# Performance work log

Hardware: AMD Instinct MI355X
Metric: run time of the kernel (lower is better)

Reference implementation:

```python
import jax, jax.numpy as jnp
import numpy as np

D_OUT, D1, D2 = 512, 512, 512
R0, R1, R2 = 128, 128, 128
BATCH = 8192


def setup_inputs() -> dict:
    key = jax.random.key(0)
    k1, k2, k3, k4, k5, k6 = jax.random.split(key, 6)
    return {
        "X1": jax.random.normal(k1, (D1, BATCH), dtype=jnp.float32),
        "X2": jax.random.normal(k2, (D2, BATCH), dtype=jnp.float32),
        "U0": jax.random.normal(k3, (D_OUT, R0), dtype=jnp.float32) * 0.05,
        "U1": jax.random.normal(k4, (D1, R1), dtype=jnp.float32) * 0.05,
        "U2": jax.random.normal(k5, (D2, R2), dtype=jnp.float32) * 0.05,
        "G": jax.random.normal(k6, (R0, R1, R2), dtype=jnp.float32) * 0.05,
    }


def reference(X1, X2, U0, U1, U2, G):
    # Per-mode projections: UX_i = U_{i+1}^T @ X_i  -> [r_i, B]
    UX1 = U1.T @ X1  # [R1, B]
    UX2 = U2.T @ X2  # [R2, B]
    # Column-wise Khatri-Rao product of UX1, UX2 gives kron per column with
    # row index q*R2 + r (C order), which matches mode-0 unfolding of G.
    # Fused form: core = G_(0) @ khatri_rao(UX1, UX2), expressed as one einsum.
    core = jnp.einsum('pqr,qb,rb->pb', G, UX1, UX2)  # [R0, B]
    Z = U0 @ core  # [D_OUT, B]
    return Z
```

## Files before the change

### kernel.cpp

```cpp
#include <hip/hip_runtime.h>
#include <hip/hip_bf16.h>
#include <stdint.h>


typedef __attribute__((ext_vector_type(8))) short bf8;
typedef __attribute__((ext_vector_type(4))) short bf4;
typedef __attribute__((ext_vector_type(4))) float f4;

__device__ __forceinline__ unsigned short f2bf(float f){
  unsigned x = __builtin_bit_cast(unsigned, f);
  x += 0x7fffu + ((x >> 16) & 1u);
  return (unsigned short)(x >> 16);
}
__device__ __forceinline__ float bf2f(unsigned short u){
  unsigned x = ((unsigned)u) << 16;
  return __builtin_bit_cast(float, x);
}
__device__ __forceinline__ void glds16(const void* g, void* l){
  __builtin_amdgcn_global_load_lds(
      (const __attribute__((address_space(1))) void*)g,
      (__attribute__((address_space(3))) void*)l, 16, 0, 0);
}

__global__ __launch_bounds__(256) void k_cast(const float* __restrict__ G,
                                              const float* __restrict__ U0,
                                              const float* __restrict__ U1,
                                              const float* __restrict__ U2,
                                              unsigned short* __restrict__ Gbf,
                                              unsigned short* __restrict__ U0bf,
                                              unsigned short* __restrict__ U1T,
                                              unsigned short* __restrict__ U2T){
  const int blk = blockIdx.x;
  if (blk < 2112){
    const int i4 = blk * 256 + threadIdx.x;
    const int NG4 = 2097152 / 4;
    const float4* src; unsigned short* dst; int j4;
    if (i4 < NG4){ src = (const float4*)G;  dst = Gbf;  j4 = i4; }
    else         { src = (const float4*)U0; dst = U0bf; j4 = i4 - NG4; }
    float4 v = src[j4];
    ushort4 o = make_ushort4(f2bf(v.x), f2bf(v.y), f2bf(v.z), f2bf(v.w));
    ((ushort4*)dst)[j4] = o;
  } else {
    const int b2 = blk - 2112;
    const float* U = (b2 < 256) ? U1 : U2;
    unsigned short* UT = (b2 < 256) ? U1T : U2T;
    const int idx = (b2 & 255) * 256 + threadIdx.x;
    const int d = idx >> 7, q = idx & 127;
    UT[q * 512 + d] = f2bf(U[idx]);
  }
}

__global__ __launch_bounds__(256) void k_ux2(const unsigned short* __restrict__ U1T,
                                             const unsigned short* __restrict__ U2T,
                                             const float* __restrict__ X1,
                                             const float* __restrict__ X2,
                                             float* __restrict__ OUTF,
                                             unsigned short* __restrict__ OUTT){
  const bool second = (blockIdx.y != 0);
  const unsigned short* UT = second ? U2T : U1T;
  const float* X = second ? X2 : X1;
  __shared__ __align__(16) unsigned char lds[16384 + 8192];
  unsigned char* ldsA = lds;
  unsigned char* ldsB = lds + 16384;
  const int tid = threadIdx.x, lane = tid & 63, wv = tid >> 6;
  const int wr = wv >> 1, wc = wv & 1;
  const int b0 = blockIdx.x * 64;
  f4 acc[4][2] = {};

  for (int it = 0; it < 8; ++it){
    const int k0 = it * 64;
#pragma unroll
    for (int i = 0; i < 4; ++i){
      const int L = (wv * 4 + i) * 1024 + lane * 16;
      const int row = L >> 7;
      const int ss = (lane & 7) ^ (row & 7);
      glds16(UT + (size_t)row * 512 + k0 + ss * 8, ldsA + (wv * 4 + i) * 1024);
    }
#pragma unroll
    for (int c = 0; c < 2; ++c){
      const int slot = c * 4 + wv;
      const int bRow = lane;
      bf8 v;
#pragma unroll
      for (int j = 0; j < 8; ++j)
        v[j] = (short)f2bf(X[(size_t)(k0 + slot * 8 + j) * 8192 + b0 + bRow]);
      *(bf8*)(ldsB + bRow * 128 + ((slot ^ (bRow & 7)) << 4)) = v;
    }
    __syncthreads();
#pragma unroll
    for (int kc = 0; kc < 2; ++kc){
      const int g = lane >> 4;
      bf8 a[4], b[2];
#pragma unroll
      for (int mf = 0; mf < 4; ++mf){
        const int r = wr * 64 + mf * 16 + (lane & 15);
        a[mf] = *(const bf8*)(ldsA + r * 128 + (((kc * 4 + g) ^ (r & 7)) << 4));
      }
#pragma unroll
      for (int nf = 0; nf < 2; ++nf){
        const int rb = wc * 32 + nf * 16 + (lane & 15);
        b[nf] = *(const bf8*)(ldsB + rb * 128 + (((kc * 4 + g) ^ (rb & 7)) << 4));
      }
#pragma unroll
      for (int mf = 0; mf < 4; ++mf)
#pragma unroll
        for (int nf = 0; nf < 2; ++nf)
          acc[mf][nf] = __builtin_amdgcn_mfma_f32_16x16x32_bf16(a[mf], b[nf], acc[mf][nf], 0, 0, 0);
    }
    __syncthreads();
  }

  if (!second){
#pragma unroll
    for (int mf = 0; mf < 4; ++mf)
#pragma unroll
      for (int nf = 0; nf < 2; ++nf)
#pragma unroll
        for (int j = 0; j < 4; ++j){
          const int q = wr * 64 + mf * 16 + (lane >> 4) * 4 + j;
          const int b = b0 + wc * 32 + nf * 16 + (lane & 15);
          OUTF[(size_t)q * 8192 + b] = acc[mf][nf][j];
        }
  } else {
#pragma unroll
    for (int mf = 0; mf < 4; ++mf)
#pragma unroll
      for (int nf = 0; nf < 2; ++nf){
        const int rBase = wr * 64 + mf * 16 + (lane >> 4) * 4;
        const int bL = wc * 32 + nf * 16 + (lane & 15);
        bf4 p;
#pragma unroll
        for (int j = 0; j < 4; ++j) p[j] = (short)f2bf(acc[mf][nf][j]);
        *(bf4*)(lds + ((bL * 256 + rBase * 2) ^ ((bL & 7) << 4))) = p;
      }
    __syncthreads();
#pragma unroll
    for (int u = 0; u < 4; ++u){
      const int sIdx = u * 256 + tid;
      const int bL = sIdx >> 4, slot = sIdx & 15;
      bf8 v = *(const bf8*)(lds + bL * 256 + ((slot ^ (bL & 7)) << 4));
      *(bf8*)(OUTT + (size_t)(b0 + bL) * 128 + slot * 8) = v;
    }
  }
}

__global__ __launch_bounds__(512, 2) void k_core(const unsigned short* __restrict__ Gbf,
                                                 const float* __restrict__ UX1,
                                                 const unsigned short* __restrict__ UX2T,
                                                 unsigned short* __restrict__ PT){
  __shared__ __align__(16) unsigned char lds[147456];
  unsigned char* ldsX = lds + 131072;
  const int tid = threadIdx.x, lane = tid & 63, wv = tid >> 6;
  const int g = lane >> 4, l15 = lane & 15;
  const int wr = wv >> 1, wc = wv & 1;
  const int blk = blockIdx.x;
  const int xcd = blk & 7, slot = blk >> 3;
  const int split = xcd >> 1;
  const int b0 = ((xcd & 1) * 32 + slot) * 128;
  const int q0 = split * 32;

  auto stageA = [&](int q, int buf){
#pragma unroll
    for (int rnd = 0; rnd < 4; ++rnd){
      const int off = rnd * 8192 + wv * 1024 + lane * 16;
      const int row = off >> 8;
      const int ss = ((off >> 4) & 15) ^ (row & 7);
      glds16(Gbf + (size_t)row * 16384 + (size_t)q * 128 + ss * 8,
             lds + buf * 32768 + off);
    }
  };

#pragma unroll
  for (int rnd = 0; rnd < 2; ++rnd){
    const int off = rnd * 8192 + wv * 1024 + lane * 16;
    const int row = off >> 9;
    glds16(UX1 + (size_t)(q0 + row) * 8192 + b0 + ((off >> 2) & 127), ldsX + off);
  }
  bf8 Bf[4][4];
#pragma unroll
  for (int kc = 0; kc < 4; ++kc)
#pragma unroll
    for (int nf = 0; nf < 4; ++nf)
      Bf[kc][nf] = *(const bf8*)(UX2T + (size_t)(b0 + wc * 64 + nf * 16 + l15) * 128 +
                                 kc * 32 + g * 8);
  stageA(q0 + 0, 0);
  stageA(q0 + 1, 1);
  stageA(q0 + 2, 2);

  f4 acc[2][4];
#pragma unroll
  for (int mf = 0; mf < 2; ++mf)
#pragma unroll
    for (int nf = 0; nf < 4; ++nf) acc[mf][nf] = (f4){0.f, 0.f, 0.f, 0.f};

  auto bodyq = [&](int i){
    const unsigned char* A = lds + (i & 3) * 32768;
    float xs[4];
#pragma unroll
    for (int nf = 0; nf < 4; ++nf)
      xs[nf] = *(const float*)(ldsX + i * 512 + (wc * 64 + nf * 16 + l15) * 4);
    bf8 a[2][4];
#pragma unroll
    for (int mf = 0; mf < 2; ++mf){
      const int row = wr * 32 + mf * 16 + l15;
#pragma unroll
      for (int kc = 0; kc < 4; ++kc)
        a[mf][kc] = *(const bf8*)(A + row * 256 + ((((kc << 2) + g) ^ (row & 7)) << 4));
    }
#pragma unroll
    for (int mf = 0; mf < 2; ++mf)
#pragma unroll
      for (int nf = 0; nf < 4; ++nf){
        f4 y = __builtin_amdgcn_mfma_f32_16x16x32_bf16(a[mf][0], Bf[0][nf], (f4){0.f,0.f,0.f,0.f}, 0, 0, 0);
        y = __builtin_amdgcn_mfma_f32_16x16x32_bf16(a[mf][1], Bf[1][nf], y, 0, 0, 0);
        y = __builtin_amdgcn_mfma_f32_16x16x32_bf16(a[mf][2], Bf[2][nf], y, 0, 0, 0);
        y = __builtin_amdgcn_mfma_f32_16x16x32_bf16(a[mf][3], Bf[3][nf], y, 0, 0, 0);
        acc[mf][nf] += y * xs[nf];
      }
  };

  for (int i = 0; i < 30; ++i){
    asm volatile("s_waitcnt vmcnt(8)" ::: "memory");
    __builtin_amdgcn_s_barrier();
    stageA(q0 + i + 3, (i + 3) & 3);
    bodyq(i);
  }
  asm volatile("s_waitcnt vmcnt(4)" ::: "memory");
  __builtin_amdgcn_s_barrier();
  bodyq(30);
  asm volatile("s_waitcnt vmcnt(0)" ::: "memory");
  __builtin_amdgcn_s_barrier();
  bodyq(31);

  __syncthreads();
#pragma unroll
  for (int mf = 0; mf < 2; ++mf)
#pragma unroll
    for (int nf = 0; nf < 4; ++nf){
      const int bL = wc * 64 + nf * 16 + l15;
      const int pq = wr * 8 + mf * 4 + g;
      *(f4*)(lds + bL * 512 + ((pq ^ (bL & 7)) << 4)) = acc[mf][nf];
    }
  __syncthreads();
#pragma unroll
  for (int rnd = 0; rnd < 4; ++rnd){
    const int idx = rnd * 512 + tid;
    const int bL = idx >> 4, s8 = idx & 15;
    f4 lo = *(const f4*)(lds + bL * 512 + (((s8 * 2) ^ (bL & 7)) << 4));
    f4 hi = *(const f4*)(lds + bL * 512 + (((s8 * 2 + 1) ^ (bL & 7)) << 4));
    bf8 o;
#pragma unroll
    for (int j = 0; j < 4; ++j){
      o[j] = (short)f2bf(lo[j]);
      o[4 + j] = (short)f2bf(hi[j]);
    }
    *(bf8*)(PT + (size_t)split * 1048576 + (size_t)(b0 + bL) * 128 + s8 * 8) = o;
  }
}

__global__ __launch_bounds__(256) void k_red(const unsigned short* __restrict__ PT,
                                             unsigned short* __restrict__ coreT){
  const int c = blockIdx.x * 256 + threadIdx.x;
  const bf8* P = (const bf8*)PT;
  bf8 v0 = P[c], v1 = P[c + 131072], v2 = P[c + 262144], v3 = P[c + 393216];
  bf8 o;
#pragma unroll
  for (int j = 0; j < 8; ++j){
    float s = bf2f((unsigned short)v0[j]) + bf2f((unsigned short)v1[j]) +
              bf2f((unsigned short)v2[j]) + bf2f((unsigned short)v3[j]);
    o[j] = (short)f2bf(s);
  }
  ((bf8*)coreT)[c] = o;
}

__global__ __launch_bounds__(256) void k_z(const unsigned short* __restrict__ U0bf,
                                           const unsigned short* __restrict__ coreT,
                                           float* __restrict__ Z){
  __shared__ __align__(16) unsigned char lds[32768];
  unsigned char* ldsA = lds;
  unsigned char* ldsB = lds + 16384;
  const int tid = threadIdx.x, lane = tid & 63, wv = tid >> 6;
  const int wr = wv >> 1, wc = wv & 1;
  const int b0 = blockIdx.x * 128;
  const int d0 = blockIdx.y * 128;
  f4 acc[4][4] = {};

#pragma unroll
  for (int it = 0; it < 2; ++it){
    const int k0 = it * 64;
#pragma unroll
    for (int i = 0; i < 4; ++i){
      const int L = (wv * 4 + i) * 1024 + lane * 16;
      const int row = L >> 7;
      const int ss = (lane & 7) ^ (row & 7);
      glds16(U0bf + (size_t)(d0 + row) * 128 + k0 + ss * 8, ldsA + (wv * 4 + i) * 1024);
      glds16(coreT + (size_t)(b0 + row) * 128 + k0 + ss * 8, ldsB + (wv * 4 + i) * 1024);
    }
    __syncthreads();
#pragma unroll
    for (int kc = 0; kc < 2; ++kc){
      const int g = lane >> 4;
      bf8 a[4], b[4];
#pragma unroll
      for (int mf = 0; mf < 4; ++mf){
        const int r = wr * 64 + mf * 16 + (lane & 15);
        a[mf] = *(const bf8*)(ldsA + r * 128 + (((kc * 4 + g) ^ (r & 7)) << 4));
      }
#pragma unroll
      for (int nf = 0; nf < 4; ++nf){
        const int rb = wc * 64 + nf * 16 + (lane & 15);
        b[nf] = *(const bf8*)(ldsB + rb * 128 + (((kc * 4 + g) ^ (rb & 7)) << 4));
      }
#pragma unroll
      for (int mf = 0; mf < 4; ++mf)
#pragma unroll
        for (int nf = 0; nf < 4; ++nf)
          acc[mf][nf] = __builtin_amdgcn_mfma_f32_16x16x32_bf16(a[mf], b[nf], acc[mf][nf], 0, 0, 0);
    }
    __syncthreads();
  }
#pragma unroll
  for (int mf = 0; mf < 4; ++mf)
#pragma unroll
    for (int nf = 0; nf < 4; ++nf)
#pragma unroll
      for (int j = 0; j < 4; ++j){
        const int d = d0 + wr * 64 + mf * 16 + (lane >> 4) * 4 + j;
        const int b = b0 + wc * 64 + nf * 16 + (lane & 15);
        Z[(size_t)d * 8192 + b] = acc[mf][nf][j];
      }
}

extern "C" void kernel_launch(void* const* d_in, const int* in_sizes, int n_in,
                              void* d_out, int out_size, void* d_ws, size_t ws_size,
                              hipStream_t stream){
  const float* X1 = (const float*)d_in[0];
  const float* X2 = (const float*)d_in[1];
  const float* U0 = (const float*)d_in[2];
  const float* U1 = (const float*)d_in[3];
  const float* U2 = (const float*)d_in[4];
  const float* G  = (const float*)d_in[5];
  float* Z = (float*)d_out;

  char* ws = (char*)d_ws;
  unsigned short* Gbf   = (unsigned short*)(ws);
  unsigned short* U0bf  = (unsigned short*)(ws + 4194304);
  unsigned short* U1T   = (unsigned short*)(ws + 4325376);
  unsigned short* U2T   = (unsigned short*)(ws + 4456448);
  float*          UX1   = (float*)         (ws + 4587520);
  unsigned short* UX2T  = (unsigned short*)(ws + 8781824);
  unsigned short* coreT = (unsigned short*)(ws + 10878976);
  unsigned short* PT    = (unsigned short*)(ws + 12976128);

  k_cast<<<dim3(2624), dim3(256), 0, stream>>>(G, U0, U1, U2, Gbf, U0bf, U1T, U2T);
  k_ux2 <<<dim3(128, 2), dim3(256), 0, stream>>>(U1T, U2T, X1, X2, UX1, UX2T);
  k_core<<<dim3(256), dim3(512), 0, stream>>>(Gbf, UX1, UX2T, PT);
  k_red <<<dim3(512), dim3(256), 0, stream>>>(PT, coreT);
  k_z   <<<dim3(64, 4), dim3(256), 0, stream>>>(U0bf, coreT, Z);
}
```

Baseline: 70.06 us.

## Give each core wave a private G ring, drop block barriers, split q eightfold

Restructures k_core so each of 4 waves owns 32 rows of p and stages its own double-buffered G slices. This removes the block-wide s_barrier from every q step, and UX1 scalars are read straight from global memory instead of an LDS stage. The q range is split across 8 blocks instead of 4, giving 512 smaller blocks with less LDS each. Partials are rounded to bf16 before the LDS transpose, and k_red now sums 8 partial buffers. The cost is double the partial-sum write and reduce traffic, a larger PT workspace, and an extra bf16 rounding step on the partials.

```diff
diff --git a/kernel.cpp b/kernel.cpp
--- a/kernel.cpp
+++ b/kernel.cpp
@@ -144,73 +144,68 @@
   }
 }
 
-__global__ __launch_bounds__(512, 2) void k_core(const unsigned short* __restrict__ Gbf,
+__global__ __launch_bounds__(256, 2) void k_core(const unsigned short* __restrict__ Gbf,
                                                  const float* __restrict__ UX1,
                                                  const unsigned short* __restrict__ UX2T,
                                                  unsigned short* __restrict__ PT){
-  __shared__ __align__(16) unsigned char lds[147456];
-  unsigned char* ldsX = lds + 131072;
+  __shared__ __align__(16) unsigned char lds[65536];
   const int tid = threadIdx.x, lane = tid & 63, wv = tid >> 6;
   const int g = lane >> 4, l15 = lane & 15;
-  const int wr = wv >> 1, wc = wv & 1;
   const int blk = blockIdx.x;
-  const int xcd = blk & 7, slot = blk >> 3;
-  const int split = xcd >> 1;
-  const int b0 = ((xcd & 1) * 32 + slot) * 128;
-  const int q0 = split * 32;
+  const int split = blk & 7;
+  const int b0 = (blk >> 3) * 128;
+  const int q0 = split * 16;
+  const int p0 = wv * 32;
+  unsigned char* ring = lds + wv * 16384;
 
   auto stageA = [&](int q, int buf){
-#pragma unroll
-    for (int rnd = 0; rnd < 4; ++rnd){
-      const int off = rnd * 8192 + wv * 1024 + lane * 16;
-      const int row = off >> 8;
-      const int ss = ((off >> 4) & 15) ^ (row & 7);
-      glds16(Gbf + (size_t)row * 16384 + (size_t)q * 128 + ss * 8,
-             lds + buf * 32768 + off);
+    unsigned char* dst = ring + buf * 8192;
+#pragma unroll
+    for (int j = 0; j < 8; ++j){
+      const int row = j * 4 + g;
+      const int ss = l15 ^ (row & 7);
+      glds16(Gbf + (size_t)(p0 + row) * 16384 + (size_t)q * 128 + ss * 8,
+             dst + j * 1024);
     }
   };
 
-#pragma unroll
-  for (int rnd = 0; rnd < 2; ++rnd){
-    const int off = rnd * 8192 + wv * 1024 + lane * 16;
-    const int row = off >> 9;
-    glds16(UX1 + (size_t)(q0 + row) * 8192 + b0 + ((off >> 2) & 127), ldsX + off);
-  }
-  bf8 Bf[4][4];
+  bf8 Bf[4][8];
 #pragma unroll
   for (int kc = 0; kc < 4; ++kc)
 #pragma unroll
-    for (int nf = 0; nf < 4; ++nf)
-      Bf[kc][nf] = *(const bf8*)(UX2T + (size_t)(b0 + wc * 64 + nf * 16 + l15) * 128 +
+    for (int nf = 0; nf < 8; ++nf)
+      Bf[kc][nf] = *(const bf8*)(UX2T + (size_t)(b0 + nf * 16 + l15) * 128 +
                                  kc * 32 + g * 8);
   stageA(q0 + 0, 0);
   stageA(q0 + 1, 1);
-  stageA(q0 + 2, 2);
-
-  f4 acc[2][4];
+
+  f4 acc[2][8];
 #pragma unroll
   for (int mf = 0; mf < 2; ++mf)
 #pragma unroll
-    for (int nf = 0; nf < 4; ++nf) acc[mf][nf] = (f4){0.f, 0.f, 0.f, 0.f};
-
-  auto bodyq = [&](int i){
-    const unsigned char* A = lds + (i & 3) * 32768;
-    float xs[4];
-#pragma unroll
-    for (int nf = 0; nf < 4; ++nf)
-      xs[nf] = *(const float*)(ldsX + i * 512 + (wc * 64 + nf * 16 + l15) * 4);
+    for (int nf = 0; nf < 8; ++nf) acc[mf][nf] = (f4){0.f, 0.f, 0.f, 0.f};
+
+  auto iter = [&](int i, bool stage_next){
+    const unsigned char* A = ring + (i & 1) * 8192;
+    float xs[8];
+#pragma unroll
+    for (int nf = 0; nf < 8; ++nf)
+      xs[nf] = UX1[(size_t)(q0 + i) * 8192 + b0 + nf * 16 + l15];
     bf8 a[2][4];
 #pragma unroll
     for (int mf = 0; mf < 2; ++mf){
-      const int row = wr * 32 + mf * 16 + l15;
+      const int row = mf * 16 + l15;
 #pragma unroll
       for (int kc = 0; kc < 4; ++kc)
         a[mf][kc] = *(const bf8*)(A + row * 256 + ((((kc << 2) + g) ^ (row & 7)) << 4));
     }
+    asm volatile("s_waitcnt lgkmcnt(0)" ::: "memory");
+    __builtin_amdgcn_sched_barrier(0);
+    if (stage_next) stageA(q0 + i + 2, i & 1);
 #pragma unroll
     for (int mf = 0; mf < 2; ++mf)
 #pragma unroll
-      for (int nf = 0; nf < 4; ++nf){
+      for (int nf = 0; nf < 8; ++nf){
         f4 y = __builtin_amdgcn_mfma_f32_16x16x32_bf16(a[mf][0], Bf[0][nf], (f4){0.f,0.f,0.f,0.f}, 0, 0, 0);
         y = __builtin_amdgcn_mfma_f32_16x16x32_bf16(a[mf][1], Bf[1][nf], y, 0, 0, 0);
         y = __builtin_amdgcn_mfma_f32_16x16x32_bf16(a[mf][2], Bf[2][nf], y, 0, 0, 0);
@@ -219,41 +214,37 @@
       }
   };
 
-  for (int i = 0; i < 30; ++i){
+  for (int i = 0; i < 14; ++i){
     asm volatile("s_waitcnt vmcnt(8)" ::: "memory");
-    __builtin_amdgcn_s_barrier();
-    stageA(q0 + i + 3, (i + 3) & 3);
-    bodyq(i);
-  }
-  asm volatile("s_waitcnt vmcnt(4)" ::: "memory");
-  __builtin_amdgcn_s_barrier();
-  bodyq(30);
+    iter(i, true);
+  }
+  asm volatile("s_waitcnt vmcnt(8)" ::: "memory");
+  iter(14, false);
   asm volatile("s_waitcnt vmcnt(0)" ::: "memory");
-  __builtin_amdgcn_s_barrier();
-  bodyq(31);
+  iter(15, false);
 
   __syncthreads();
 #pragma unroll
   for (int mf = 0; mf < 2; ++mf)
 #pragma unroll
-    for (int nf = 0; nf < 4; ++nf){
-      const int bL = wc * 64 + nf * 16 + l15;
-      const int pq = wr * 8 + mf * 4 + g;
-      *(f4*)(lds + bL * 512 + ((pq ^ (bL & 7)) << 4)) = acc[mf][nf];
+    for (int nf = 0; nf < 8; ++nf){
+      const int bL = nf * 16 + l15;
+      const int pq = wv * 8 + mf * 4 + g;
+      bf4 o;
+#pragma unroll
+      for (int j = 0; j < 4; ++j) o[j] = (short)f2bf(acc[mf][nf][j]);
+      *(bf4*)(lds + bL * 256 + ((pq ^ (bL & 7)) << 3)) = o;
     }
   __syncthreads();
 #pragma unroll
-  for (int rnd = 0; rnd < 4; ++rnd){
-    const int idx = rnd * 512 + tid;
+  for (int rnd = 0; rnd < 8; ++rnd){
+    const int idx = rnd * 256 + tid;
     const int bL = idx >> 4, s8 = idx & 15;
-    f4 lo = *(const f4*)(lds + bL * 512 + (((s8 * 2) ^ (bL & 7)) << 4));
-    f4 hi = *(const f4*)(lds + bL * 512 + (((s8 * 2 + 1) ^ (bL & 7)) << 4));
+    bf4 lo = *(const bf4*)(lds + bL * 256 + (((s8 * 2) ^ (bL & 7)) << 3));
+    bf4 hi = *(const bf4*)(lds + bL * 256 + (((s8 * 2 + 1) ^ (bL & 7)) << 3));
     bf8 o;
 #pragma unroll
-    for (int j = 0; j < 4; ++j){
-      o[j] = (short)f2bf(lo[j]);
-      o[4 + j] = (short)f2bf(hi[j]);
-    }
+    for (int j = 0; j < 4; ++j){ o[j] = lo[j]; o[4 + j] = hi[j]; }
     *(bf8*)(PT + (size_t)split * 1048576 + (size_t)(b0 + bL) * 128 + s8 * 8) = o;
   }
 }
@@ -262,14 +253,16 @@
                                              unsigned short* __restrict__ coreT){
   const int c = blockIdx.x * 256 + threadIdx.x;
   const bf8* P = (const bf8*)PT;
-  bf8 v0 = P[c], v1 = P[c + 131072], v2 = P[c + 262144], v3 = P[c + 393216];
+  float s[8] = {};
+#pragma unroll
+  for (int sp = 0; sp < 8; ++sp){
+    bf8 v = P[c + sp * 131072];
+#pragma unroll
+    for (int j = 0; j < 8; ++j) s[j] += bf2f((unsigned short)v[j]);
+  }
   bf8 o;
 #pragma unroll
-  for (int j = 0; j < 8; ++j){
-    float s = bf2f((unsigned short)v0[j]) + bf2f((unsigned short)v1[j]) +
-              bf2f((unsigned short)v2[j]) + bf2f((unsigned short)v3[j]);
-    o[j] = (short)f2bf(s);
-  }
+  for (int j = 0; j < 8; ++j) o[j] = (short)f2bf(s[j]);
   ((bf8*)coreT)[c] = o;
 }
 
@@ -354,7 +347,7 @@
 
   k_cast<<<dim3(2624), dim3(256), 0, stream>>>(G, U0, U1, U2, Gbf, U0bf, U1T, U2T);
   k_ux2 <<<dim3(128, 2), dim3(256), 0, stream>>>(U1T, U2T, X1, X2, UX1, UX2T);
-  k_core<<<dim3(256), dim3(512), 0, stream>>>(Gbf, UX1, UX2T, PT);
+  k_core<<<dim3(512), dim3(256), 0, stream>>>(Gbf, UX1, UX2T, PT);
   k_red <<<dim3(512), dim3(256), 0, stream>>>(PT, coreT);
   k_z   <<<dim3(64, 4), dim3(256), 0, stream>>>(U0bf, coreT, Z);
 }
```

Result: slower. 73.41 us (+4.8%).

## Retile core contraction to 256-column blocks with 8-way q split and phased pipeline

Applied to the files above, without the earlier changes.

The core kernel now processes 256 batch columns per block with an 8-way split over q (16 q each) instead of 128 columns with a 4-way split. Each wave computes 64 rows, and each q step is split into two phases with interleaved G staging, setprio around the MFMAs, and triple buffering in place of quadruple. Partial results are converted to bf16 before the LDS transpose. The aim is better reuse of G tiles per block and more overlap of loads with MFMA work, at the cost of writing and reducing twice as many partial-sum buffers in the reduction kernel.

```diff
diff --git a/kernel.cpp b/kernel.cpp
--- a/kernel.cpp
+++ b/kernel.cpp
@@ -148,34 +148,24 @@
                                                  const float* __restrict__ UX1,
                                                  const unsigned short* __restrict__ UX2T,
                                                  unsigned short* __restrict__ PT){
-  __shared__ __align__(16) unsigned char lds[147456];
-  unsigned char* ldsX = lds + 131072;
+  __shared__ __align__(16) unsigned char lds[114688];
+  unsigned char* ldsX = lds + 98304;
   const int tid = threadIdx.x, lane = tid & 63, wv = tid >> 6;
   const int g = lane >> 4, l15 = lane & 15;
-  const int wr = wv >> 1, wc = wv & 1;
+  const int wr = wv >> 2, wc = wv & 3;
   const int blk = blockIdx.x;
-  const int xcd = blk & 7, slot = blk >> 3;
-  const int split = xcd >> 1;
-  const int b0 = ((xcd & 1) * 32 + slot) * 128;
-  const int q0 = split * 32;
-
-  auto stageA = [&](int q, int buf){
-#pragma unroll
-    for (int rnd = 0; rnd < 4; ++rnd){
-      const int off = rnd * 8192 + wv * 1024 + lane * 16;
-      const int row = off >> 8;
-      const int ss = ((off >> 4) & 15) ^ (row & 7);
-      glds16(Gbf + (size_t)row * 16384 + (size_t)q * 128 + ss * 8,
-             lds + buf * 32768 + off);
-    }
+  const int split = blk & 7;
+  const int b0 = (blk >> 3) * 256;
+  const int q0 = split * 16;
+
+  auto stageA = [&](int q, int buf, int rnd){
+    const int off = rnd * 8192 + wv * 1024 + lane * 16;
+    const int row = off >> 8;
+    const int ss = ((off >> 4) & 15) ^ (row & 7);
+    glds16(Gbf + (size_t)row * 16384 + (size_t)q * 128 + ss * 8,
+           lds + buf * 32768 + off);
   };
 
-#pragma unroll
-  for (int rnd = 0; rnd < 2; ++rnd){
-    const int off = rnd * 8192 + wv * 1024 + lane * 16;
-    const int row = off >> 9;
-    glds16(UX1 + (size_t)(q0 + row) * 8192 + b0 + ((off >> 2) & 127), ldsX + off);
-  }
   bf8 Bf[4][4];
 #pragma unroll
   for (int kc = 0; kc < 4; ++kc)
@@ -183,77 +173,110 @@
     for (int nf = 0; nf < 4; ++nf)
       Bf[kc][nf] = *(const bf8*)(UX2T + (size_t)(b0 + wc * 64 + nf * 16 + l15) * 128 +
                                  kc * 32 + g * 8);
-  stageA(q0 + 0, 0);
-  stageA(q0 + 1, 1);
-  stageA(q0 + 2, 2);
-
-  f4 acc[2][4];
-#pragma unroll
-  for (int mf = 0; mf < 2; ++mf)
+#pragma unroll
+  for (int rnd = 0; rnd < 2; ++rnd){
+    const int off = rnd * 8192 + wv * 1024 + lane * 16;
+    const int row = off >> 10;
+    glds16(UX1 + (size_t)(q0 + row) * 8192 + b0 + ((off >> 2) & 255), ldsX + off);
+  }
+#pragma unroll
+  for (int rnd = 0; rnd < 4; ++rnd) stageA(q0, 0, rnd);
+#pragma unroll
+  for (int rnd = 0; rnd < 4; ++rnd) stageA(q0 + 1, 1, rnd);
+
+  f4 acc[4][4];
+#pragma unroll
+  for (int mf = 0; mf < 4; ++mf)
 #pragma unroll
     for (int nf = 0; nf < 4; ++nf) acc[mf][nf] = (f4){0.f, 0.f, 0.f, 0.f};
-
-  auto bodyq = [&](int i){
-    const unsigned char* A = lds + (i & 3) * 32768;
-    float xs[4];
-#pragma unroll
-    for (int nf = 0; nf < 4; ++nf)
-      xs[nf] = *(const float*)(ldsX + i * 512 + (wc * 64 + nf * 16 + l15) * 4);
-    bf8 a[2][4];
-#pragma unroll
-    for (int mf = 0; mf < 2; ++mf){
-      const int row = wr * 32 + mf * 16 + l15;
-#pragma unroll
-      for (int kc = 0; kc < 4; ++kc)
-        a[mf][kc] = *(const bf8*)(A + row * 256 + ((((kc << 2) + g) ^ (row & 7)) << 4));
-    }
-#pragma unroll
-    for (int mf = 0; mf < 2; ++mf)
-#pragma unroll
-      for (int nf = 0; nf < 4; ++nf){
-        f4 y = __builtin_amdgcn_mfma_f32_16x16x32_bf16(a[mf][0], Bf[0][nf], (f4){0.f,0.f,0.f,0.f}, 0, 0, 0);
-        y = __builtin_amdgcn_mfma_f32_16x16x32_bf16(a[mf][1], Bf[1][nf], y, 0, 0, 0);
-        y = __builtin_amdgcn_mfma_f32_16x16x32_bf16(a[mf][2], Bf[2][nf], y, 0, 0, 0);
-        y = __builtin_amdgcn_mfma_f32_16x16x32_bf16(a[mf][3], Bf[3][nf], y, 0, 0, 0);
-        acc[mf][nf] += y * xs[nf];
-      }
-  };
-
-  for (int i = 0; i < 30; ++i){
-    asm volatile("s_waitcnt vmcnt(8)" ::: "memory");
-    __builtin_amdgcn_s_barrier();
-    stageA(q0 + i + 3, (i + 3) & 3);
-    bodyq(i);
-  }
+  float xs[4];
+
   asm volatile("s_waitcnt vmcnt(4)" ::: "memory");
   __builtin_amdgcn_s_barrier();
-  bodyq(30);
-  asm volatile("s_waitcnt vmcnt(0)" ::: "memory");
-  __builtin_amdgcn_s_barrier();
-  bodyq(31);
+
+  auto phase = [&](int i, const unsigned char* A, int ph, bool doStage,
+                   int stq, int sbuf, int vm){
+    bf8 a[2][4];
+#pragma unroll
+    for (int mfp = 0; mfp < 2; ++mfp){
+      const int row = wr * 64 + (ph * 2 + mfp) * 16 + l15;
+#pragma unroll
+      for (int kc = 0; kc < 4; ++kc)
+        a[mfp][kc] = *(const bf8*)(A + row * 256 + ((((kc << 2) + g) ^ (row & 7)) << 4));
+    }
+    if (ph == 0){
+#pragma unroll
+      for (int nf = 0; nf < 4; ++nf)
+        xs[nf] = *(const float*)(ldsX + i * 1024 + (wc * 64 + nf * 16 + l15) * 4);
+    }
+    if (doStage){ stageA(stq, sbuf, ph * 2); stageA(stq, sbuf, ph * 2 + 1); }
+    __builtin_amdgcn_s_barrier();
+    asm volatile("s_waitcnt lgkmcnt(0)" ::: "memory");
+    __builtin_amdgcn_sched_barrier(0);
+    __builtin_amdgcn_s_setprio(1);
+    f4 y[2][4];
+#pragma unroll
+    for (int mfp = 0; mfp < 2; ++mfp)
+#pragma unroll
+      for (int nf = 0; nf < 4; ++nf){
+        f4 t = __builtin_amdgcn_mfma_f32_16x16x32_bf16(a[mfp][0], Bf[0][nf], (f4){0.f,0.f,0.f,0.f}, 0, 0, 0);
+        t = __builtin_amdgcn_mfma_f32_16x16x32_bf16(a[mfp][1], Bf[1][nf], t, 0, 0, 0);
+        t = __builtin_amdgcn_mfma_f32_16x16x32_bf16(a[mfp][2], Bf[2][nf], t, 0, 0, 0);
+        y[mfp][nf] = __builtin_amdgcn_mfma_f32_16x16x32_bf16(a[mfp][3], Bf[3][nf], t, 0, 0, 0);
+      }
+    __builtin_amdgcn_s_setprio(0);
+#pragma unroll
+    for (int mfp = 0; mfp < 2; ++mfp)
+#pragma unroll
+      for (int nf = 0; nf < 4; ++nf)
+        acc[ph * 2 + mfp][nf] += y[mfp][nf] * xs[nf];
+    if (vm == 4)      asm volatile("s_waitcnt vmcnt(4)" ::: "memory");
+    else if (vm == 0) asm volatile("s_waitcnt vmcnt(0)" ::: "memory");
+    __builtin_amdgcn_s_barrier();
+  };
+
+  int cur = 0;
+  for (int i = 0; i < 14; ++i){
+    const unsigned char* A = lds + cur * 32768;
+    int sbuf = cur + 2; if (sbuf >= 3) sbuf -= 3;
+    phase(i, A, 0, true, q0 + i + 2, sbuf, -1);
+    phase(i, A, 1, true, q0 + i + 2, sbuf, 4);
+    ++cur; if (cur == 3) cur = 0;
+  }
+  {
+    const unsigned char* A = lds + cur * 32768;
+    phase(14, A, 0, false, 0, 0, -1);
+    phase(14, A, 1, false, 0, 0, 0);
+    ++cur; if (cur == 3) cur = 0;
+  }
+  {
+    const unsigned char* A = lds + cur * 32768;
+    phase(15, A, 0, false, 0, 0, -1);
+    phase(15, A, 1, false, 0, 0, -1);
+  }
 
   __syncthreads();
 #pragma unroll
-  for (int mf = 0; mf < 2; ++mf)
+  for (int mf = 0; mf < 4; ++mf)
 #pragma unroll
     for (int nf = 0; nf < 4; ++nf){
       const int bL = wc * 64 + nf * 16 + l15;
-      const int pq = wr * 8 + mf * 4 + g;
-      *(f4*)(lds + bL * 512 + ((pq ^ (bL & 7)) << 4)) = acc[mf][nf];
+      const int pq = wr * 16 + mf * 4 + g;
+      bf4 o;
+#pragma unroll
+      for (int j = 0; j < 4; ++j) o[j] = (short)f2bf(acc[mf][nf][j]);
+      *(bf4*)(lds + bL * 256 + ((pq ^ (bL & 7)) << 3)) = o;
     }
   __syncthreads();
 #pragma unroll
-  for (int rnd = 0; rnd < 4; ++rnd){
+  for (int rnd = 0; rnd < 8; ++rnd){
     const int idx = rnd * 512 + tid;
     const int bL = idx >> 4, s8 = idx & 15;
-    f4 lo = *(const f4*)(lds + bL * 512 + (((s8 * 2) ^ (bL & 7)) << 4));
-    f4 hi = *(const f4*)(lds + bL * 512 + (((s8 * 2 + 1) ^ (bL & 7)) << 4));
+    bf4 lo = *(const bf4*)(lds + bL * 256 + (((s8 * 2) ^ (bL & 7)) << 3));
+    bf4 hi = *(const bf4*)(lds + bL * 256 + (((s8 * 2 + 1) ^ (bL & 7)) << 3));
     bf8 o;
 #pragma unroll
-    for (int j = 0; j < 4; ++j){
-      o[j] = (short)f2bf(lo[j]);
-      o[4 + j] = (short)f2bf(hi[j]);
-    }
+    for (int j = 0; j < 4; ++j){ o[j] = lo[j]; o[4 + j] = hi[j]; }
     *(bf8*)(PT + (size_t)split * 1048576 + (size_t)(b0 + bL) * 128 + s8 * 8) = o;
   }
 }
@@ -262,14 +285,16 @@
                                              unsigned short* __restrict__ coreT){
   const int c = blockIdx.x * 256 + threadIdx.x;
   const bf8* P = (const bf8*)PT;
-  bf8 v0 = P[c], v1 = P[c + 131072], v2 = P[c + 262144], v3 = P[c + 393216];
+  float s[8] = {};
+#pragma unroll
+  for (int sp = 0; sp < 8; ++sp){
+    bf8 v = P[c + sp * 131072];
+#pragma unroll
+    for (int j = 0; j < 8; ++j) s[j] += bf2f((unsigned short)v[j]);
+  }
   bf8 o;
 #pragma unroll
-  for (int j = 0; j < 8; ++j){
-    float s = bf2f((unsigned short)v0[j]) + bf2f((unsigned short)v1[j]) +
-              bf2f((unsigned short)v2[j]) + bf2f((unsigned short)v3[j]);
-    o[j] = (short)f2bf(s);
-  }
+  for (int j = 0; j < 8; ++j) o[j] = (short)f2bf(s[j]);
   ((bf8*)coreT)[c] = o;
 }
 
```

Result: no change. 71.11 us (+1.5%).
